# Performance work log

Hardware: AMD Instinct MI355X
Metric: run time of the kernel (lower is better)

## Reference

```python
import jax, jax.numpy as jnp
import numpy as np
from jax import lax

N, IN_CH, OUT_CH, KERNEL, D = 16, 256, 256, 3, 4096
FACTOR = 2  # upsampling factor
RESAMPLE_K = (1.0, 3.0, 3.0, 1.0)


def _fir_kernel():
    # _setup_kernel: normalize to sum 1; upsample path scales by gain * factor
    k = np.asarray(RESAMPLE_K, dtype=np.float32)
    k = k / k.sum()
    return k * FACTOR  # gain = 1


def setup_inputs() -> dict:
    key = jax.random.key(0)
    k1, k2, k3 = jax.random.split(key, 3)
    x = jax.random.normal(k1, (N, IN_CH, D), dtype=jnp.float32)
    weight = jax.random.normal(k2, (OUT_CH, IN_CH, KERNEL), dtype=jnp.float32) * 0.05
    bias = jax.random.normal(k3, (OUT_CH,), dtype=jnp.float32) * 0.05
    return {"x": x, "weight": weight, "bias": bias}


def _upfirdn1d(x, k, pad0, pad1):
    # up=down=1 path of StyleGAN2 upfirdn1d: pad, then TRUE convolution with FIR k
    # (torch native impl flips k before F.conv1d). Depthwise via [N*C,1,L] reshape.
    n, c, _ = x.shape
    xp = jnp.pad(x, ((0, 0), (0, 0), (pad0, pad1)))
    kr = k[::-1][None, None, :]  # flip -> correlation == convolution
    y = lax.conv_general_dilated(
        xp.reshape(n * c, 1, -1), kr, window_strides=(1,), padding=[(0, 0)],
        dimension_numbers=("NCH", "OIH", "NCH"))
    return y.reshape(n, c, -1)


def _upsample_conv_1d(x, w):
    # torch: w reshaped/flipped/permuted then conv_transpose1d(stride=factor).
    # conv_transpose with that transformed weight == correlation with the ORIGINAL
    # w on an input dilated by `factor` with (convH-1) padding on both sides
    # (output_padding = 0 for these shapes).
    convH = w.shape[2]
    y = lax.conv_general_dilated(
        x, w, window_strides=(1,), padding=[(convH - 1, convH - 1)],
        lhs_dilation=(FACTOR,), dimension_numbers=("NCH", "OIH", "NCH"))
    k = jnp.asarray(_fir_kernel())
    p = k.shape[0] - FACTOR - (convH - 1)  # = 0 here
    pad0 = (p + 1) // 2 + FACTOR - 1
    pad1 = p // 2 + 1
    return _upfirdn1d(y, k, pad0, pad1)  # -> [N, C_out, D * FACTOR]


def reference(x, weight, bias):
    y = _upsample_conv_1d(x, weight)
    return y + bias[None, :, None]
```

## Files before the change

### kernel.cpp

```cpp
#include <hip/hip_runtime.h>
#include <hip/hip_bf16.h>

#define N_   16
#define CI_  256
#define CO_  256
#define D_   4096
#define DO_  8192
#define KTOT 768
#define XTROWS 4098
#define WT_ELEMS (512 * KTOT)
#define XT_ELEMS ((size_t)N_ * XTROWS * 256)

typedef short frag8 __attribute__((ext_vector_type(8)));
typedef float facc4 __attribute__((ext_vector_type(4)));

static __device__ __forceinline__ unsigned short f2bf(float f) {
    union { __hip_bfloat16 h; unsigned short u; } cv;
    cv.h = __float2bfloat16(f);
    return cv.u;
}

static __device__ __forceinline__ unsigned int pack2(float lo, float hi) {
    return (unsigned int)f2bf(lo) | ((unsigned int)f2bf(hi) << 16);
}

static __device__ __forceinline__ void async16(unsigned short* lds, const unsigned short* g) {
    __builtin_amdgcn_global_load_lds(
        (const __attribute__((address_space(1))) unsigned int*)g,
        (__attribute__((address_space(3))) unsigned int*)lds, 16, 0, 0);
}

#define DSREAD(dst, a, litoff) \
    asm volatile("ds_read_b128 %0, %1 offset:" litoff : "=&v"(dst) : "v"(a))

__global__ __launch_bounds__(256) void prep_wt(const float* __restrict__ w,
                                               unsigned short* __restrict__ Wt) {
    const int ci = threadIdx.x;
    const int co = blockIdx.x;
    const float* wp = w + ((size_t)co * CI_ + ci) * 3;
    const float w0 = wp[0], w1 = wp[1], w2 = wp[2];
    const float e0 = 0.25f * w1 + 0.75f * w0;
    const float e1 = 0.75f * w2 + 0.75f * w1 + 0.25f * w0;
    const float e2 = 0.25f * w2;
    const float o0 = 0.25f * w0;
    const float o1 = 0.25f * w2 + 0.75f * w1 + 0.75f * w0;
    const float o2 = 0.75f * w2 + 0.25f * w1;
    unsigned short* pe = Wt + (size_t)(co * 2 + 0) * KTOT;
    unsigned short* po = Wt + (size_t)(co * 2 + 1) * KTOT;
    pe[0 * 256 + ci] = f2bf(e0); pe[1 * 256 + ci] = f2bf(e1); pe[2 * 256 + ci] = f2bf(e2);
    po[0 * 256 + ci] = f2bf(o0); po[1 * 256 + ci] = f2bf(o1); po[2 * 256 + ci] = f2bf(o2);
}

__global__ __launch_bounds__(256) void prep_xt2(const float* __restrict__ x,
                                                unsigned short* __restrict__ xt) {
    __shared__ unsigned int Lp[32][133];
    const int tid = threadIdx.x;
    const int t0  = blockIdx.x * 32;
    const int n   = blockIdx.y;
    const float* xn = x + (size_t)n * CI_ * D_;
    unsigned short* slab = xt + (size_t)n * XTROWS * 256;

    if (t0 == 0 && tid < 128)       ((unsigned int*)slab)[tid] = 0u;
    if (t0 == D_ - 32 && tid < 128) ((unsigned int*)(slab + (size_t)(XTROWS - 1) * 256))[tid] = 0u;

    const int cp_l  = tid >> 3;
    const int t_off = (tid & 7) * 4;

    #pragma unroll
    for (int p = 0; p < 4; ++p) {
        const int ci0 = p * 64 + cp_l * 2;
        float4 a = *(const float4*)(xn + (size_t)ci0 * D_ + t0 + t_off);
        float4 b = *(const float4*)(xn + (size_t)(ci0 + 1) * D_ + t0 + t_off);
        const int cp = p * 32 + cp_l;
        Lp[t_off + 0][cp] = pack2(a.x, b.x);
        Lp[t_off + 1][cp] = pack2(a.y, b.y);
        Lp[t_off + 2][cp] = pack2(a.z, b.z);
        Lp[t_off + 3][cp] = pack2(a.w, b.w);
    }
    __syncthreads();

    #pragma unroll
    for (int it = 0; it < 4; ++it) {
        const int row = it * 8 + (tid >> 5);
        const int c4  = (tid & 31) * 4;
        uint4 v;
        v.x = Lp[row][c4 + 0];
        v.y = Lp[row][c4 + 1];
        v.z = Lp[row][c4 + 2];
        v.w = Lp[row][c4 + 3];
        *(uint4*)(slab + (size_t)(1 + t0 + row) * 256 + c4 * 2) = v;
    }
}

__global__ __launch_bounds__(256) void gemm_upfir(
    const unsigned short* __restrict__ Wt, const unsigned short* __restrict__ xt,
    const float* __restrict__ bias, float* __restrict__ out)
{
    __shared__ __align__(16) unsigned short As[3][128 * 32];
    __shared__ __align__(16) unsigned short Bs[3][128 * 32];

    const int tid  = threadIdx.x;
    const int lane = tid & 63;
    const int wid  = tid >> 6;
    const int quad = lane >> 4;
    const int l16  = lane & 15;

    const int bt0 = blockIdx.x * 128;
    const int bm0 = blockIdx.y * 128;
    const int n   = blockIdx.z;

    const int srow = lane >> 2;
    const int slot = lane & 3;
    const unsigned short* gsrc;
    int lds_off;
    int ginc;
    if (wid < 2) {
        int row0 = wid * 64 + srow;
        int cg   = slot ^ ((row0 >> 1) & 3);
        gsrc    = Wt + (size_t)(bm0 + row0) * KTOT + cg * 8;
        lds_off = wid * 2048;
        ginc    = 16 * KTOT;
    } else {
        int row0 = (wid - 2) * 64 + srow;
        int cg   = slot ^ ((row0 >> 1) & 3);
        gsrc    = xt + (size_t)n * XTROWS * 256 + (size_t)(bt0 + row0) * 256 + cg * 8;
        lds_off = (wid - 2) * 2048;
        ginc    = 16 * 256;
    }

    const int swz = quad ^ ((l16 >> 1) & 3);
    const int wave_m = (wid & 1) * 64;
    const int wave_t = (wid >> 1) * 64;

    const unsigned baseA = (unsigned)(size_t)&As[0][0];
    const unsigned baseB = (unsigned)(size_t)&Bs[0][0];
    const unsigned plA = baseA + (unsigned)(((wave_m + l16) * 32 + swz * 8) * 2);
    const unsigned plB = baseB + (unsigned)(((wave_t + l16) * 32 + swz * 8) * 2);

    facc4 acc[4][4] = {};

    {
        unsigned short* s0 = (wid < 2 ? As[0] : Bs[0]) + lds_off;
        unsigned short* s1 = (wid < 2 ? As[1] : Bs[1]) + lds_off;
        #pragma unroll
        for (int i = 0; i < 4; ++i) async16(s0 + i * 512, gsrc + (size_t)i * ginc);
        #pragma unroll
        for (int i = 0; i < 4; ++i) async16(s1 + i * 512, gsrc + (size_t)i * ginc + 32);
    }

    #pragma unroll
    for (int s = 0; s < 24; ++s) {
        const int bc = s % 3;
        const int bn = (s + 2) % 3;
        if (s < 23) asm volatile("s_waitcnt vmcnt(4)" ::: "memory");
        else        asm volatile("s_waitcnt vmcnt(0)" ::: "memory");
        __builtin_amdgcn_s_barrier();

        const unsigned ab = plA + (unsigned)(bc * 8192);
        const unsigned bb = plB + (unsigned)(bc * 8192);
        frag8 af[4], bfr[4];
        DSREAD(bfr[0], bb, "0");
        DSREAD(bfr[1], bb, "1024");
        DSREAD(bfr[2], bb, "2048");
        DSREAD(bfr[3], bb, "3072");
        DSREAD(af[0],  ab, "0");
        DSREAD(af[1],  ab, "1024");
        DSREAD(af[2],  ab, "2048");
        DSREAD(af[3],  ab, "3072");

        if (s + 2 < 24) {
            unsigned short* sb = (wid < 2 ? As[bn] : Bs[bn]) + lds_off;
            #pragma unroll
            for (int i = 0; i < 4; ++i)
                async16(sb + i * 512, gsrc + (size_t)i * ginc + (size_t)(s + 2) * 32);
        }

        __builtin_amdgcn_s_setprio(1);
        #define MFMA_GROUP(mi, lit)                                              \
            asm volatile("s_waitcnt lgkmcnt(" lit ")" ::: "memory");             \
            __builtin_amdgcn_sched_barrier(0);                                   \
            acc[mi][0] = __builtin_amdgcn_mfma_f32_16x16x32_bf16(af[mi], bfr[0], acc[mi][0], 0, 0, 0); \
            acc[mi][1] = __builtin_amdgcn_mfma_f32_16x16x32_bf16(af[mi], bfr[1], acc[mi][1], 0, 0, 0); \
            acc[mi][2] = __builtin_amdgcn_mfma_f32_16x16x32_bf16(af[mi], bfr[2], acc[mi][2], 0, 0, 0); \
            acc[mi][3] = __builtin_amdgcn_mfma_f32_16x16x32_bf16(af[mi], bfr[3], acc[mi][3], 0, 0, 0);
        MFMA_GROUP(0, "3")
        MFMA_GROUP(1, "2")
        MFMA_GROUP(2, "1")
        MFMA_GROUP(3, "0")
        #undef MFMA_GROUP
        __builtin_amdgcn_s_setprio(0);
    }

    #pragma unroll
    for (int mi = 0; mi < 4; ++mi) {
        int m0  = bm0 + wave_m + mi * 16 + quad * 4;
        int co0 = m0 >> 1;
        float b0 = bias[co0];
        float b1 = bias[co0 + 1];
        #pragma unroll
        for (int ti = 0; ti < 4; ++ti) {
            int t = bt0 + wave_t + ti * 16 + l16;
            facc4 v = acc[mi][ti];
            float* p0 = out + ((size_t)(n * CO_ + co0)) * DO_ + 2 * t;
            float* p1 = p0 + DO_;
            *(float2*)p0 = make_float2(v.x + b0, v.y + b0);
            *(float2*)p1 = make_float2(v.z + b1, v.w + b1);
        }
    }
}

__global__ __launch_bounds__(256) void upconv_fir_f32(
    const float* __restrict__ x, const float* __restrict__ w,
    const float* __restrict__ bias, float* __restrict__ out)
{
    __shared__ float ws[CI_][4];
    const int tid = threadIdx.x;
    const int co  = blockIdx.y;
    const int n   = blockIdx.z;
    {
        const float* wc = w + (size_t)co * CI_ * 3;
        ws[tid][0] = wc[tid * 3 + 0];
        ws[tid][1] = wc[tid * 3 + 1];
        ws[tid][2] = wc[tid * 3 + 2];
        ws[tid][3] = 0.f;
    }
    __syncthreads();
    const int t0 = (blockIdx.x * 256 + tid) * 8;
    const float* xn = x + (size_t)n * CI_ * D_;
    float s[10], g[9];
    #pragma unroll
    for (int k = 0; k < 10; ++k) s[k] = 0.f;
    #pragma unroll
    for (int k = 0; k < 9; ++k) g[k] = 0.f;
    #pragma unroll 2
    for (int ci = 0; ci < CI_; ++ci) {
        const float* xr = xn + ci * D_;
        float4 va = *(const float4*)(xr + t0);
        float4 vb = *(const float4*)(xr + t0 + 4);
        float  xm = (t0 > 0)      ? xr[t0 - 1] : 0.f;
        float  xp = (t0 + 8 < D_) ? xr[t0 + 8] : 0.f;
        float4 wv = *(const float4*)(&ws[ci][0]);
        const float w0 = wv.x, w1 = wv.y, w2 = wv.z;
        float xa[10];
        xa[0] = xm; xa[1] = va.x; xa[2] = va.y; xa[3] = va.z; xa[4] = va.w;
        xa[5] = vb.x; xa[6] = vb.y; xa[7] = vb.z; xa[8] = vb.w; xa[9] = xp;
        #pragma unroll
        for (int k = 0; k < 10; ++k) s[k] += w1 * xa[k];
        #pragma unroll
        for (int k = 0; k < 9; ++k)  g[k] += w0 * xa[k] + w2 * xa[k + 1];
    }
    const float b = bias[co];
    float o16[16];
    #pragma unroll
    for (int tt = 0; tt < 8; ++tt) {
        o16[2 * tt]     = 0.25f * (s[tt] + g[tt + 1]) + 0.75f * (g[tt] + s[tt + 1]) + b;
        o16[2 * tt + 1] = 0.25f * (g[tt] + s[tt + 2]) + 0.75f * (s[tt + 1] + g[tt + 1]) + b;
    }
    float* ob = out + ((size_t)n * CO_ + co) * DO_ + 2 * t0;
    *(float4*)(ob + 0)  = make_float4(o16[0],  o16[1],  o16[2],  o16[3]);
    *(float4*)(ob + 4)  = make_float4(o16[4],  o16[5],  o16[6],  o16[7]);
    *(float4*)(ob + 8)  = make_float4(o16[8],  o16[9],  o16[10], o16[11]);
    *(float4*)(ob + 12) = make_float4(o16[12], o16[13], o16[14], o16[15]);
}

extern "C" void kernel_launch(void* const* d_in, const int* in_sizes, int n_in,
                              void* d_out, int out_size, void* d_ws, size_t ws_size,
                              hipStream_t stream) {
    const float* x  = (const float*)d_in[0];
    const float* w  = (const float*)d_in[1];
    const float* b  = (const float*)d_in[2];
    float* out      = (float*)d_out;

    const size_t need = (size_t)WT_ELEMS * 2 + XT_ELEMS * 2;
    if (ws_size >= need) {
        unsigned short* Wt = (unsigned short*)d_ws;
        unsigned short* xt = Wt + WT_ELEMS;
        prep_wt<<<dim3(CO_), 256, 0, stream>>>(w, Wt);
        prep_xt2<<<dim3(D_ / 32, N_), 256, 0, stream>>>(x, xt);
        gemm_upfir<<<dim3(D_ / 128, 4, N_), 256, 0, stream>>>(Wt, xt, b, out);
    } else {
        upconv_fir_f32<<<dim3(2, CO_, N_), 256, 0, stream>>>(x, w, b, out);
    }
}
```

Baseline: 238.4 us.

## Enlarge GEMM M tile to 256 rows per block with 128x64 per-wave tiles

Doubles the block tile along the output-channel/phase dimension from 128 to 256. Each wave now computes 128x64 outputs with an 8x4 MFMA accumulator grid, and all four waves cooperatively issue loads for both the A and B slabs. The goal is more MFMA work per LDS B-fragment load and less redundant reloading of the x tile across blocks. In exchange it doubles accumulator registers, raises LDS usage, and halves the grid, which may lower occupancy and leave fewer blocks to hide latency.

```diff
diff --git a/kernel.cpp b/kernel.cpp
--- a/kernel.cpp
+++ b/kernel.cpp
@@ -96,7 +96,7 @@
     const unsigned short* __restrict__ Wt, const unsigned short* __restrict__ xt,
     const float* __restrict__ bias, float* __restrict__ out)
 {
-    __shared__ __align__(16) unsigned short As[3][128 * 32];
+    __shared__ __align__(16) unsigned short As[3][256 * 32];
     __shared__ __align__(16) unsigned short Bs[3][128 * 32];
 
     const int tid  = threadIdx.x;
@@ -106,59 +106,55 @@
     const int l16  = lane & 15;
 
     const int bt0 = blockIdx.x * 128;
-    const int bm0 = blockIdx.y * 128;
+    const int bm0 = blockIdx.y * 256;
     const int n   = blockIdx.z;
 
     const int srow = lane >> 2;
     const int slot = lane & 3;
-    const unsigned short* gsrc;
-    int lds_off;
-    int ginc;
-    if (wid < 2) {
-        int row0 = wid * 64 + srow;
-        int cg   = slot ^ ((row0 >> 1) & 3);
-        gsrc    = Wt + (size_t)(bm0 + row0) * KTOT + cg * 8;
-        lds_off = wid * 2048;
-        ginc    = 16 * KTOT;
-    } else {
-        int row0 = (wid - 2) * 64 + srow;
-        int cg   = slot ^ ((row0 >> 1) & 3);
-        gsrc    = xt + (size_t)n * XTROWS * 256 + (size_t)(bt0 + row0) * 256 + cg * 8;
-        lds_off = (wid - 2) * 2048;
-        ginc    = 16 * 256;
-    }
+    const int cg   = slot ^ ((srow >> 1) & 3);
+    const unsigned short* gA = Wt + (size_t)(bm0 + wid * 64 + srow) * KTOT + cg * 8;
+    const unsigned short* gB = xt + (size_t)n * XTROWS * 256
+                                  + (size_t)(bt0 + wid * 32 + srow) * 256 + cg * 8;
+    const int ldsA = (wid * 64) * 32;
+    const int ldsB = (wid * 32) * 32;
 
     const int swz = quad ^ ((l16 >> 1) & 3);
-    const int wave_m = (wid & 1) * 64;
-    const int wave_t = (wid >> 1) * 64;
+    const int wm  = (wid & 1) * 128;
+    const int wt  = (wid >> 1) * 64;
 
     const unsigned baseA = (unsigned)(size_t)&As[0][0];
     const unsigned baseB = (unsigned)(size_t)&Bs[0][0];
-    const unsigned plA = baseA + (unsigned)(((wave_m + l16) * 32 + swz * 8) * 2);
-    const unsigned plB = baseB + (unsigned)(((wave_t + l16) * 32 + swz * 8) * 2);
-
-    facc4 acc[4][4] = {};
-
-    {
-        unsigned short* s0 = (wid < 2 ? As[0] : Bs[0]) + lds_off;
-        unsigned short* s1 = (wid < 2 ? As[1] : Bs[1]) + lds_off;
-        #pragma unroll
-        for (int i = 0; i < 4; ++i) async16(s0 + i * 512, gsrc + (size_t)i * ginc);
-        #pragma unroll
-        for (int i = 0; i < 4; ++i) async16(s1 + i * 512, gsrc + (size_t)i * ginc + 32);
-    }
+    const unsigned plA = baseA + (unsigned)(((wm + l16) * 32 + swz * 8) * 2);
+    const unsigned plB = baseB + (unsigned)(((wt + l16) * 32 + swz * 8) * 2);
+
+    facc4 acc[8][4] = {};
+
+    #define STAGE(b, s)                                                          \
+        do {                                                                     \
+            unsigned short* da = &As[b][0] + ldsA;                               \
+            unsigned short* db = &Bs[b][0] + ldsB;                               \
+            async16(da + 0 * 512, gA + (size_t)0 * 16 * KTOT + (s) * 32);        \
+            async16(da + 1 * 512, gA + (size_t)1 * 16 * KTOT + (s) * 32);        \
+            async16(da + 2 * 512, gA + (size_t)2 * 16 * KTOT + (s) * 32);        \
+            async16(da + 3 * 512, gA + (size_t)3 * 16 * KTOT + (s) * 32);        \
+            async16(db + 0 * 512, gB + (size_t)0 * 16 * 256 + (s) * 32);         \
+            async16(db + 1 * 512, gB + (size_t)1 * 16 * 256 + (s) * 32);         \
+        } while (0)
+
+    STAGE(0, 0);
+    STAGE(1, 1);
 
     #pragma unroll
     for (int s = 0; s < 24; ++s) {
         const int bc = s % 3;
         const int bn = (s + 2) % 3;
-        if (s < 23) asm volatile("s_waitcnt vmcnt(4)" ::: "memory");
+        if (s < 23) asm volatile("s_waitcnt vmcnt(6)" ::: "memory");
         else        asm volatile("s_waitcnt vmcnt(0)" ::: "memory");
         __builtin_amdgcn_s_barrier();
 
-        const unsigned ab = plA + (unsigned)(bc * 8192);
+        const unsigned ab = plA + (unsigned)(bc * 16384);
         const unsigned bb = plB + (unsigned)(bc * 8192);
-        frag8 af[4], bfr[4];
+        frag8 af[8], bfr[4];
         DSREAD(bfr[0], bb, "0");
         DSREAD(bfr[1], bb, "1024");
         DSREAD(bfr[2], bb, "2048");
@@ -167,40 +163,44 @@
         DSREAD(af[1],  ab, "1024");
         DSREAD(af[2],  ab, "2048");
         DSREAD(af[3],  ab, "3072");
-
-        if (s + 2 < 24) {
-            unsigned short* sb = (wid < 2 ? As[bn] : Bs[bn]) + lds_off;
-            #pragma unroll
-            for (int i = 0; i < 4; ++i)
-                async16(sb + i * 512, gsrc + (size_t)i * ginc + (size_t)(s + 2) * 32);
-        }
+        DSREAD(af[4],  ab, "4096");
+        DSREAD(af[5],  ab, "5120");
+        DSREAD(af[6],  ab, "6144");
+        DSREAD(af[7],  ab, "7168");
+
+        if (s + 2 < 24) STAGE(bn, s + 2);
 
         __builtin_amdgcn_s_setprio(1);
-        #define MFMA_GROUP(mi, lit)                                              \
+        #define MFMA_GROUP(a, lit)                                               \
             asm volatile("s_waitcnt lgkmcnt(" lit ")" ::: "memory");             \
             __builtin_amdgcn_sched_barrier(0);                                   \
-            acc[mi][0] = __builtin_amdgcn_mfma_f32_16x16x32_bf16(af[mi], bfr[0], acc[mi][0], 0, 0, 0); \
-            acc[mi][1] = __builtin_amdgcn_mfma_f32_16x16x32_bf16(af[mi], bfr[1], acc[mi][1], 0, 0, 0); \
-            acc[mi][2] = __builtin_amdgcn_mfma_f32_16x16x32_bf16(af[mi], bfr[2], acc[mi][2], 0, 0, 0); \
-            acc[mi][3] = __builtin_amdgcn_mfma_f32_16x16x32_bf16(af[mi], bfr[3], acc[mi][3], 0, 0, 0);
-        MFMA_GROUP(0, "3")
-        MFMA_GROUP(1, "2")
-        MFMA_GROUP(2, "1")
-        MFMA_GROUP(3, "0")
+            acc[a][0] = __builtin_amdgcn_mfma_f32_16x16x32_bf16(af[a], bfr[0], acc[a][0], 0, 0, 0); \
+            acc[a][1] = __builtin_amdgcn_mfma_f32_16x16x32_bf16(af[a], bfr[1], acc[a][1], 0, 0, 0); \
+            acc[a][2] = __builtin_amdgcn_mfma_f32_16x16x32_bf16(af[a], bfr[2], acc[a][2], 0, 0, 0); \
+            acc[a][3] = __builtin_amdgcn_mfma_f32_16x16x32_bf16(af[a], bfr[3], acc[a][3], 0, 0, 0);
+        MFMA_GROUP(0, "7")
+        MFMA_GROUP(1, "6")
+        MFMA_GROUP(2, "5")
+        MFMA_GROUP(3, "4")
+        MFMA_GROUP(4, "3")
+        MFMA_GROUP(5, "2")
+        MFMA_GROUP(6, "1")
+        MFMA_GROUP(7, "0")
         #undef MFMA_GROUP
         __builtin_amdgcn_s_setprio(0);
     }
-
-    #pragma unroll
-    for (int mi = 0; mi < 4; ++mi) {
-        int m0  = bm0 + wave_m + mi * 16 + quad * 4;
+    #undef STAGE
+
+    #pragma unroll
+    for (int a = 0; a < 8; ++a) {
+        int m0  = bm0 + wm + a * 16 + quad * 4;
         int co0 = m0 >> 1;
         float b0 = bias[co0];
         float b1 = bias[co0 + 1];
         #pragma unroll
-        for (int ti = 0; ti < 4; ++ti) {
-            int t = bt0 + wave_t + ti * 16 + l16;
-            facc4 v = acc[mi][ti];
+        for (int b = 0; b < 4; ++b) {
+            int t = bt0 + wt + b * 16 + l16;
+            facc4 v = acc[a][b];
             float* p0 = out + ((size_t)(n * CO_ + co0)) * DO_ + 2 * t;
             float* p1 = p0 + DO_;
             *(float2*)p0 = make_float2(v.x + b0, v.y + b0);
@@ -277,7 +277,7 @@
         unsigned short* xt = Wt + WT_ELEMS;
         prep_wt<<<dim3(CO_), 256, 0, stream>>>(w, Wt);
         prep_xt2<<<dim3(D_ / 32, N_), 256, 0, stream>>>(x, xt);
-        gemm_upfir<<<dim3(D_ / 128, 4, N_), 256, 0, stream>>>(Wt, xt, b, out);
+        gemm_upfir<<<dim3(D_ / 128, 2, N_), 256, 0, stream>>>(Wt, xt, b, out);
     } else {
         upconv_fir_f32<<<dim3(2, CO_, N_), 256, 0, stream>>>(x, w, b, out);
     }
```

Result: no change. 241.2 us (+1.2%).
